# Performance work log

Hardware: AMD Instinct MI355X
Metric: run time of the kernel (lower is better)

The kernel has to match this reference:

```python
import jax, jax.numpy as jnp
import numpy as np
from jax import lax

K = 3      # kernel_size
PAD = 1    # padding
OG = 2     # offset groups


def _conv2d(x, w, b):
    y = lax.conv_general_dilated(x, w, (1, 1), [(PAD, PAD), (PAD, PAD)],
                                 dimension_numbers=('NCHW', 'OIHW', 'NCHW'))
    return y + b[None, :, None, None]


def _deform_conv2d(x, offset, mask, weight):
    # torchvision-style modulated deform_conv2d (v2), stride=1, dilation=1,
    # zero out-of-bounds, offset layout [B, OG*K*K*2, H, W] with (dy, dx) pairs.
    B, C, H, W = x.shape
    O = weight.shape[0]
    K2 = K * K
    Cg = C // OG

    ki, kj = jnp.meshgrid(jnp.arange(K), jnp.arange(K), indexing='ij')
    ki = ki.reshape(K2)
    kj = kj.reshape(K2)
    base_y = jnp.arange(H)[None, :] - PAD + ki[:, None]   # [K2, H]
    base_x = jnp.arange(W)[None, :] - PAD + kj[:, None]   # [K2, W]

    off = offset.reshape(B, OG, K2, 2, H, W)
    py = off[:, :, :, 0] + base_y[None, None, :, :, None].astype(x.dtype)  # [B,OG,K2,H,W]
    px = off[:, :, :, 1] + base_x[None, None, :, None, :].astype(x.dtype)
    m = mask.reshape(B, OG, K2, H, W)

    y0f = jnp.floor(py)
    x0f = jnp.floor(px)
    wy1 = py - y0f   # bilinear weights, grads flow through py/px
    wx1 = px - x0f
    y0 = y0f.astype(jnp.int32)
    x0 = x0f.astype(jnp.int32)
    y1 = y0 + 1
    x1 = x0 + 1

    img = x.reshape(B, OG, Cg, H * W)

    def gather(yi, xi):
        valid = (yi >= 0) & (yi < H) & (xi >= 0) & (xi < W)
        idx = jnp.clip(yi, 0, H - 1) * W + jnp.clip(xi, 0, W - 1)          # [B,OG,K2,H,W]
        v = jnp.take_along_axis(img[:, :, :, None, :],
                                idx.reshape(B, OG, 1, K2, H * W), axis=-1)
        return v.reshape(B, OG, Cg, K2, H, W) * valid[:, :, None].astype(x.dtype)

    v00 = gather(y0, x0)
    v01 = gather(y0, x1)
    v10 = gather(y1, x0)
    v11 = gather(y1, x1)

    wy1e = wy1[:, :, None]   # [B,OG,1,K2,H,W]
    wx1e = wx1[:, :, None]
    val = (v00 * (1 - wy1e) * (1 - wx1e)
           + v01 * (1 - wy1e) * wx1e
           + v10 * wy1e * (1 - wx1e)
           + v11 * wy1e * wx1e)
    val = val * m[:, :, None]                               # modulation mask

    wr = weight.reshape(O, OG, Cg, K2)
    return jnp.einsum('ogck,bgckhw->bohw', wr, val)


def setup_inputs() -> dict:
    key = jax.random.key(0)
    k1, k2, k3, k4, k5 = jax.random.split(key, 5)
    B, C, O, H, W = 4, 64, 64, 128, 128
    K2 = K * K
    x = jax.random.normal(k1, (B, C, H, W), dtype=jnp.float32)
    w_main = jax.random.normal(k2, (O, C, K, K), dtype=jnp.float32) / np.sqrt(C * K2)
    w_off = jax.random.normal(k3, (2 * OG * K2, C, K, K), dtype=jnp.float32) * 0.01
    b_off = jax.random.normal(k4, (2 * OG * K2,), dtype=jnp.float32) * 0.01
    w_mask = jnp.full((OG * K2, C, K, K), 0.5, dtype=jnp.float32)  # init_mask = 0.5
    b_mask = jax.random.normal(k5, (OG * K2,), dtype=jnp.float32) * 0.01
    return {"x": x, "w_main": w_main, "w_off": w_off, "b_off": b_off,
            "w_mask": w_mask, "b_mask": b_mask}


def reference(x, w_main, w_off, b_off, w_mask, b_mask):
    offset = _conv2d(x, w_off, b_off)
    mask = jax.nn.sigmoid(_conv2d(x, w_mask, b_mask))
    return _deform_conv2d(x, offset, mask, w_main)
```

## Files before the change

kernel.cpp:

```cpp
#include <hip/hip_runtime.h>
#include <math.h>

#define BB 4
#define C 64
#define O 64
#define H 128
#define W 128
#define K2 9
#define HW (H*W)
#define NOFF 36

typedef __bf16 bf16;
typedef bf16 bf16x8 __attribute__((ext_vector_type(8)));
typedef float f32x4 __attribute__((ext_vector_type(4)));
typedef unsigned short u16x8 __attribute__((ext_vector_type(8)));

#define BSTR 55
#define VAL_BYTES 12288
#define BUF_BYTES (64*BSTR*4)
#define SMEM_BYTES (VAL_BYTES + BUF_BYTES)
#define WFRAG 18432
#define NW_TOTAL 73728

__device__ inline unsigned short f2h_bits(float f) {
  _Float16 h = (_Float16)f;
  return __builtin_bit_cast(unsigned short, h);
}
__device__ inline float h2f(unsigned short u) {
  return (float)__builtin_bit_cast(_Float16, u);
}

__global__ __launch_bounds__(256) void prep_all(
    const float* __restrict__ x, const float* __restrict__ w_main,
    const float* __restrict__ w_off, const float* __restrict__ w_mask,
    unsigned short* __restrict__ xT16, bf16* __restrict__ wfC,
    bf16* __restrict__ wfM) {
  __shared__ float tile[64][68];
  int tid = threadIdx.x;
  int b = blockIdx.x >> 8;
  int p0 = (blockIdx.x & 255) * 64;
#pragma unroll
  for (int it = 0; it < 4; ++it) {
    int c = it * 16 + (tid >> 4);
    int p4 = (tid & 15) * 4;
    *(f32x4*)&tile[c][p4] =
        *(const f32x4*)(x + (size_t)(b * C + c) * HW + p0 + p4);
  }
  __syncthreads();
#pragma unroll
  for (int it = 0; it < 2; ++it) {
    int t = it * 256 + tid;
    int p = t >> 3;
    int h8 = t & 7;
    u16x8 o;
#pragma unroll
    for (int j = 0; j < 8; ++j) {
      bf16 v = (bf16)tile[h8 * 8 + j][p];
      o[j] = __builtin_bit_cast(unsigned short, v);
    }
    *(u16x8*)&xT16[(size_t)(b * HW + p0 + p) * C + h8 * 8] = o;
  }
  int i = blockIdx.x * 256 + tid;
  if (i < NW_TOTAL) {
    int which = (i >= 36864);
    int ii = which ? i - 36864 : i;
    int j = ii & 7;
    int l = (ii >> 3) & 63;
    int rest = ii >> 9;
    int to = rest & 3;
    int kk = (rest >> 2) % 9;
    int ph = (rest >> 2) / 9;
    int m = to * 16 + (l & 15);
    int u = kk * 32 + (l >> 4) * 8 + j;
    int tap = u >> 5;
    int c1 = u & 31;
    if (!which) {
      int c = ph * 32 + c1;
      float v = (m < NOFF) ? w_off[(m * C + c) * K2 + tap]
                : (m < 54) ? w_mask[((m - NOFF) * C + c) * K2 + tap]
                           : 0.f;
      wfC[ii] = (bf16)v;
    } else {
      wfM[ii] = (bf16)w_main[(m * C + ph * 32 + c1) * K2 + tap];
    }
  }
}

__global__ __launch_bounds__(256, 6) void fused_deform(
    const bf16* __restrict__ xT, const bf16* __restrict__ wfC,
    const bf16* __restrict__ wfM, const float* __restrict__ b_off,
    const float* __restrict__ b_mask, float* __restrict__ out) {
  __shared__ __align__(16) char smem[SMEM_BYTES];
  bf16* val = (bf16*)smem;
  unsigned int (*buf)[BSTR] = (unsigned int (*)[BSTR])(smem + VAL_BYTES);
  float* bufF = (float*)(smem + VAL_BYTES);
  bf16x8* stage16 = (bf16x8*)(smem + VAL_BYTES);
  const bf16* stageb = (const bf16*)(smem + VAL_BYTES);
  float* valF = (float*)smem;

  const int tid = threadIdx.x;
  const int lane = tid & 63;
  const int wv = tid >> 6;
  const int n16 = lane & 15;
  const int q4 = lane >> 4;
  const int chunk = tid & 3;
  const int pg = tid >> 2;
  const int row = wv * 16 + n16;

  const int g8 = blockIdx.x & 7;
  const int slot = blockIdx.x >> 3;
  const int b = g8 >> 1;
  const int ti = (g8 & 1) * 128 + slot;
  const int h0 = ti >> 1;
  const int w0 = (ti & 1) * 64;
  const bf16* xb = xT + (size_t)b * HW * C;

  bf16x8 zero8;
#pragma unroll
  for (int j = 0; j < 8; ++j) zero8[j] = (bf16)0.f;

  f32x4 accC[4] = {{0.f,0.f,0.f,0.f},{0.f,0.f,0.f,0.f},
                   {0.f,0.f,0.f,0.f},{0.f,0.f,0.f,0.f}};
#pragma unroll 1
  for (int ph = 0; ph < 2; ++ph) {
    if (ph) __syncthreads();
#pragma unroll
    for (int it = 0; it < 4; ++it) {
      int id = it * 256 + tid;
      if (id < 816) {
        int q2 = id & 3;
        int wp = (id >> 2) % 68;
        int r = (id >> 2) / 68;
        int yy = h0 + r - 1;
        int xx = w0 + wp - 1;
        bf16x8 v = zero8;
        if ((unsigned)yy < (unsigned)H && (unsigned)xx < (unsigned)W)
          v = *(const bf16x8*)(xb + (size_t)((yy << 7) + xx) * C + ph * 32 + q2 * 8);
        stage16[id] = v;
      }
    }
    __syncthreads();
    const bf16* wb = wfC + (size_t)ph * WFRAG;
#pragma unroll
    for (int kk = 0; kk < 9; ++kk) {
      bf16x8 bfr = *(const bf16x8*)(stageb +
          (size_t)(((kk / 3) * 68 + row + kk % 3) * 4 + q4) * 8);
#pragma unroll
      for (int to = 0; to < 4; ++to) {
        bf16x8 afr = *(const bf16x8*)(wb + (size_t)((kk * 4 + to) * 64 + lane) * 8);
        accC[to] = __builtin_amdgcn_mfma_f32_16x16x32_bf16(afr, bfr, accC[to], 0, 0, 0);
      }
    }
  }
  __syncthreads();

  {
#pragma unroll
    for (int to = 0; to < 4; ++to)
#pragma unroll
      for (int r = 0; r < 4; ++r) {
        int o = to * 16 + q4 * 4 + r;
        float a = accC[to][r];
        if (o < NOFF) {
          bufF[row * BSTR + o] = a + b_off[o];
        } else if (o < 54) {
          float s = a + b_mask[o - NOFF];
          bufF[row * BSTR + o] = 1.f / (1.f + __expf(-s));
        }
      }
  }
  __syncthreads();

  unsigned int rW0[5], rW1[5], rCo[5];
#pragma unroll
  for (int it = 0; it < 5; ++it) {
    int t = it * 256 + tid;
    if (t < 1152) {
      int p = t & 63;
      int gk = t >> 6;
      int g = gk / 9, tap = gk % 9;
      float offy = bufF[p * BSTR + 2 * gk];
      float offx = bufF[p * BSTR + 2 * gk + 1];
      float m = bufF[p * BSTR + NOFF + gk];
      float py = offy + (float)(h0 + tap / 3 - 1);
      float px = offx + (float)(w0 + p + tap % 3 - 1);
      float y0f = floorf(py), x0f = floorf(px);
      float wy1 = py - y0f, wx1 = px - x0f;
      float wy0 = 1.f - wy1, wx0 = 1.f - wx1;
      int y0 = (int)y0f, x0 = (int)x0f;
      int y1 = y0 + 1, x1 = x0 + 1;
      bool y0ok = (unsigned)y0 < (unsigned)H, y1ok = (unsigned)y1 < (unsigned)H;
      bool x0ok = (unsigned)x0 < (unsigned)W, x1ok = (unsigned)x1 < (unsigned)W;
      float w00 = (y0ok && x0ok) ? wy0 * wx0 * m : 0.f;
      float w01 = (y0ok && x1ok) ? wy0 * wx1 * m : 0.f;
      float w10 = (y1ok && x0ok) ? wy1 * wx0 * m : 0.f;
      float w11 = (y1ok && x1ok) ? wy1 * wx1 * m : 0.f;
      unsigned int y0c = (unsigned)min(max(y0, 0), H - 1);
      unsigned int y1c = (unsigned)min(max(y1, 0), H - 1);
      unsigned int x0c = (unsigned)min(max(x0, 0), W - 1);
      unsigned int x1c = (unsigned)min(max(x1, 0), W - 1);
      rW0[it] = (unsigned)f2h_bits(w00) | ((unsigned)f2h_bits(w01) << 16);
      rW1[it] = (unsigned)f2h_bits(w10) | ((unsigned)f2h_bits(w11) << 16);
      rCo[it] = y0c | (x0c << 8) | (y1c << 16) | (x1c << 24);
    }
  }
  __syncthreads();
#pragma unroll
  for (int it = 0; it < 5; ++it) {
    int t = it * 256 + tid;
    if (t < 1152) {
      int p = t & 63;
      int gk = t >> 6;
      buf[p][2 * gk] = rW0[it];
      buf[p][2 * gk + 1] = rW1[it];
      buf[p][NOFF + gk] = rCo[it];
    }
  }
  __syncthreads();

  f32x4 accM[4] = {{0.f,0.f,0.f,0.f},{0.f,0.f,0.f,0.f},
                   {0.f,0.f,0.f,0.f},{0.f,0.f,0.f,0.f}};
#pragma unroll 1
  for (int g = 0; g < 2; ++g) {
    const bf16* bb = xb + g * 32 + chunk * 8;
#pragma unroll 1
    for (int kc = 0; kc < 3; ++kc) {
      if (g || kc) __syncthreads();
#pragma unroll
      for (int t = 0; t < 3; ++t) {
        int tap = kc * 3 + t;
        int gk = g * 9 + tap;
        unsigned int wab = buf[pg][2 * gk];
        unsigned int wcd = buf[pg][2 * gk + 1];
        unsigned int pk = buf[pg][NOFF + gk];
        float w00 = h2f(wab & 0xffff), w01 = h2f(wab >> 16);
        float w10 = h2f(wcd & 0xffff), w11 = h2f(wcd >> 16);
        int r0 = (int)(pk & 255) << 7;
        int x0 = (int)((pk >> 8) & 255);
        int r1 = (int)((pk >> 16) & 255) << 7;
        int x1 = (int)(pk >> 24);
        bf16x8 v00 = *(const bf16x8*)(bb + (size_t)(r0 + x0) * C);
        bf16x8 v01 = *(const bf16x8*)(bb + (size_t)(r0 + x1) * C);
        bf16x8 v10 = *(const bf16x8*)(bb + (size_t)(r1 + x0) * C);
        bf16x8 v11 = *(const bf16x8*)(bb + (size_t)(r1 + x1) * C);
        bf16x8 res;
#pragma unroll
        for (int j = 0; j < 8; ++j) {
          float v = (float)v00[j] * w00 + (float)v01[j] * w01 +
                    (float)v10[j] * w10 + (float)v11[j] * w11;
          res[j] = (bf16)v;
        }
        *(bf16x8*)(val + ((t * 64 + pg) * 32 + chunk * 8)) = res;
      }
      __syncthreads();
      const bf16* wb = wfM + (size_t)g * WFRAG;
#pragma unroll
      for (int t = 0; t < 3; ++t) {
        int kk = kc * 3 + t;
        bf16x8 bfr = *(const bf16x8*)(val + ((t * 64 + row) * 32 + q4 * 8));
#pragma unroll
        for (int to = 0; to < 4; ++to) {
          bf16x8 afr = *(const bf16x8*)(wb + (size_t)((kk * 4 + to) * 64 + lane) * 8);
          accM[to] = __builtin_amdgcn_mfma_f32_16x16x32_bf16(afr, bfr, accM[to], 0, 0, 0);
        }
      }
    }
  }

  __syncthreads();
  {
#pragma unroll
    for (int to = 0; to < 4; ++to)
#pragma unroll
      for (int r = 0; r < 4; ++r)
        valF[(to * 16 + q4 * 4 + r) * 68 + row] = accM[to][r];
  }
  __syncthreads();
  {
    float* ob = out + (size_t)b * O * HW + (h0 << 7) + w0;
#pragma unroll
    for (int it = 0; it < 4; ++it) {
      int id = it * 256 + tid;
      int o = id >> 4, seg = id & 15;
      f32x4 v = *(f32x4*)&valF[o * 68 + seg * 4];
      *(f32x4*)&ob[(size_t)o * HW + seg * 4] = v;
    }
  }
}

extern "C" void kernel_launch(void* const* d_in, const int* in_sizes, int n_in,
                              void* d_out, int out_size, void* d_ws,
                              size_t ws_size, hipStream_t stream) {
  const float* x = (const float*)d_in[0];
  const float* w_main = (const float*)d_in[1];
  const float* w_off = (const float*)d_in[2];
  const float* b_off = (const float*)d_in[3];
  const float* w_mask = (const float*)d_in[4];
  const float* b_mask = (const float*)d_in[5];
  float* out = (float*)d_out;

  unsigned short* xT16 = (unsigned short*)d_ws;
  bf16* wfC = (bf16*)(xT16 + (size_t)BB * HW * C);
  bf16* wfM = wfC + 36864;

  prep_all<<<1024, 256, 0, stream>>>(x, w_main, w_off, w_mask, xT16, wfC, wfM);
  fused_deform<<<1024, 256, 0, stream>>>((const bf16*)xT16, wfC, wfM, b_off,
                                         b_mask, out);
}
```

Baseline: 116.9 us.

## Gather bilinear samples directly into MFMA B-fragments, drop LDS val staging

Each lane now computes the bilinear-interpolated bf16x8 samples that form its own MFMA B operand (row = pixel, q4 = channel chunk), instead of writing samples to a shared val buffer and reading them back after a barrier. This removes the val LDS region, the per-kc __syncthreads, and the write/read LDS traffic. The per-pixel sampling metadata is repacked into 16-byte u32x4 entries read with a single vector load. Smaller shared memory allows occupancy to rise to 8 blocks per CU via launch_bounds. The cost is that neighbouring lanes' gather loads no longer map to a contiguous per-thread 8-channel chunk layout, and register pressure may rise at the higher occupancy target.

Result: slower. 143.5 us (+22.7%).

```diff
diff --git a/kernel.cpp b/kernel.cpp
--- a/kernel.cpp
+++ b/kernel.cpp
@@ -14,11 +14,11 @@
 typedef bf16 bf16x8 __attribute__((ext_vector_type(8)));
 typedef float f32x4 __attribute__((ext_vector_type(4)));
 typedef unsigned short u16x8 __attribute__((ext_vector_type(8)));
+typedef unsigned int u32x4 __attribute__((ext_vector_type(4)));
 
 #define BSTR 55
-#define VAL_BYTES 12288
-#define BUF_BYTES (64*BSTR*4)
-#define SMEM_BYTES (VAL_BYTES + BUF_BYTES)
+#define B2STR 19
+#define SMEM_BYTES 19456
 #define WFRAG 18432
 #define NW_TOTAL 73728
 
@@ -86,16 +86,15 @@
   }
 }
 
-__global__ __launch_bounds__(256, 6) void fused_deform(
+__global__ __launch_bounds__(256, 8) void fused_deform(
     const bf16* __restrict__ xT, const bf16* __restrict__ wfC,
     const bf16* __restrict__ wfM, const float* __restrict__ b_off,
     const float* __restrict__ b_mask, float* __restrict__ out) {
   __shared__ __align__(16) char smem[SMEM_BYTES];
-  bf16* val = (bf16*)smem;
-  unsigned int (*buf)[BSTR] = (unsigned int (*)[BSTR])(smem + VAL_BYTES);
-  float* bufF = (float*)(smem + VAL_BYTES);
-  bf16x8* stage16 = (bf16x8*)(smem + VAL_BYTES);
-  const bf16* stageb = (const bf16*)(smem + VAL_BYTES);
+  bf16x8* stage16 = (bf16x8*)smem;
+  const bf16* stageb = (const bf16*)smem;
+  float* bufF = (float*)smem;
+  u32x4* buf2 = (u32x4*)smem;
   float* valF = (float*)smem;
 
   const int tid = threadIdx.x;
@@ -103,8 +102,6 @@
   const int wv = tid >> 6;
   const int n16 = lane & 15;
   const int q4 = lane >> 4;
-  const int chunk = tid & 3;
-  const int pg = tid >> 2;
   const int row = wv * 16 + n16;
 
   const int g8 = blockIdx.x & 7;
@@ -211,9 +208,8 @@
     if (t < 1152) {
       int p = t & 63;
       int gk = t >> 6;
-      buf[p][2 * gk] = rW0[it];
-      buf[p][2 * gk + 1] = rW1[it];
-      buf[p][NOFF + gk] = rCo[it];
+      u32x4 pk = {rW0[it], rW1[it], rCo[it], 0u};
+      buf2[p * B2STR + gk] = pk;
     }
   }
   __syncthreads();
@@ -222,47 +218,32 @@
                    {0.f,0.f,0.f,0.f},{0.f,0.f,0.f,0.f}};
 #pragma unroll 1
   for (int g = 0; g < 2; ++g) {
-    const bf16* bb = xb + g * 32 + chunk * 8;
-#pragma unroll 1
-    for (int kc = 0; kc < 3; ++kc) {
-      if (g || kc) __syncthreads();
-#pragma unroll
-      for (int t = 0; t < 3; ++t) {
-        int tap = kc * 3 + t;
-        int gk = g * 9 + tap;
-        unsigned int wab = buf[pg][2 * gk];
-        unsigned int wcd = buf[pg][2 * gk + 1];
-        unsigned int pk = buf[pg][NOFF + gk];
-        float w00 = h2f(wab & 0xffff), w01 = h2f(wab >> 16);
-        float w10 = h2f(wcd & 0xffff), w11 = h2f(wcd >> 16);
-        int r0 = (int)(pk & 255) << 7;
-        int x0 = (int)((pk >> 8) & 255);
-        int r1 = (int)((pk >> 16) & 255) << 7;
-        int x1 = (int)(pk >> 24);
-        bf16x8 v00 = *(const bf16x8*)(bb + (size_t)(r0 + x0) * C);
-        bf16x8 v01 = *(const bf16x8*)(bb + (size_t)(r0 + x1) * C);
-        bf16x8 v10 = *(const bf16x8*)(bb + (size_t)(r1 + x0) * C);
-        bf16x8 v11 = *(const bf16x8*)(bb + (size_t)(r1 + x1) * C);
-        bf16x8 res;
-#pragma unroll
-        for (int j = 0; j < 8; ++j) {
-          float v = (float)v00[j] * w00 + (float)v01[j] * w01 +
-                    (float)v10[j] * w10 + (float)v11[j] * w11;
-          res[j] = (bf16)v;
-        }
-        *(bf16x8*)(val + ((t * 64 + pg) * 32 + chunk * 8)) = res;
-      }
-      __syncthreads();
-      const bf16* wb = wfM + (size_t)g * WFRAG;
-#pragma unroll
-      for (int t = 0; t < 3; ++t) {
-        int kk = kc * 3 + t;
-        bf16x8 bfr = *(const bf16x8*)(val + ((t * 64 + row) * 32 + q4 * 8));
-#pragma unroll
-        for (int to = 0; to < 4; ++to) {
-          bf16x8 afr = *(const bf16x8*)(wb + (size_t)((kk * 4 + to) * 64 + lane) * 8);
-          accM[to] = __builtin_amdgcn_mfma_f32_16x16x32_bf16(afr, bfr, accM[to], 0, 0, 0);
-        }
+    const bf16* bb = xb + g * 32 + q4 * 8;
+    const bf16* wb = wfM + (size_t)g * WFRAG;
+#pragma unroll 3
+    for (int tap = 0; tap < 9; ++tap) {
+      u32x4 t4 = buf2[row * B2STR + g * 9 + tap];
+      float w00 = h2f(t4.x & 0xffff), w01 = h2f(t4.x >> 16);
+      float w10 = h2f(t4.y & 0xffff), w11 = h2f(t4.y >> 16);
+      int r0 = (int)(t4.z & 255) << 7;
+      int x0 = (int)((t4.z >> 8) & 255);
+      int r1 = (int)((t4.z >> 16) & 255) << 7;
+      int x1 = (int)(t4.z >> 24);
+      bf16x8 v00 = *(const bf16x8*)(bb + (size_t)(r0 + x0) * C);
+      bf16x8 v01 = *(const bf16x8*)(bb + (size_t)(r0 + x1) * C);
+      bf16x8 v10 = *(const bf16x8*)(bb + (size_t)(r1 + x0) * C);
+      bf16x8 v11 = *(const bf16x8*)(bb + (size_t)(r1 + x1) * C);
+      bf16x8 bfr;
+#pragma unroll
+      for (int j = 0; j < 8; ++j) {
+        float v = (float)v00[j] * w00 + (float)v01[j] * w01 +
+                  (float)v10[j] * w10 + (float)v11[j] * w11;
+        bfr[j] = (bf16)v;
+      }
+#pragma unroll
+      for (int to = 0; to < 4; ++to) {
+        bf16x8 afr = *(const bf16x8*)(wb + (size_t)((tap * 4 + to) * 64 + lane) * 8);
+        accM[to] = __builtin_amdgcn_mfma_f32_16x16x32_bf16(afr, bfr, accM[to], 0, 0, 0);
       }
     }
   }
```
